# Kernel tuning notes

Hardware: AMD Instinct MI355X
Metric: run time of the kernel (lower is better)

## Reference

```python
import jax, jax.numpy as jnp
import numpy as np

B, N, K, D, H, FF, L, NH = 8, 50, 20, 3, 128, 2048, 3, 8
S = N * K
HD = H // NH


def setup_inputs() -> dict:
    key = jax.random.key(0)
    ks = jax.random.split(key, 16)
    visited = jax.random.uniform(ks[0], (B, S)) < 0.05
    # the single most-recent action per batch row (status flips 0 -> 1)
    action_idx = jax.random.randint(ks[1], (B,), 0, S)
    visited = visited.at[jnp.arange(B), action_idx].set(True)
    feats = jax.random.normal(ks[2], (B, S, D - 1)) * visited[:, :, None]
    state = jnp.concatenate([feats, visited[:, :, None].astype(jnp.float32)], axis=-1)
    prev_state = state.at[jnp.arange(B), action_idx, :].set(0.0)

    def w(k, shape, s=0.02):
        return jax.random.normal(k, shape, dtype=jnp.float32) * s

    return dict(
        prev_state=prev_state, state=state,
        W_pre=w(ks[3], (D, H)), b_pre=jnp.zeros(H),
        Wq=w(ks[4], (L, H, H)), bq=jnp.zeros((L, H)),
        Wk=w(ks[5], (L, H, H)), bk=jnp.zeros((L, H)),
        Wv=w(ks[6], (L, H, H)), bv=jnp.zeros((L, H)),
        Wo=w(ks[7], (L, H, H)), bo=jnp.zeros((L, H)),
        ln1_g=jnp.ones((L, H)), ln1_b=jnp.zeros((L, H)),
        Wff1=w(ks[8], (L, H, FF)), bff1=jnp.zeros((L, FF)),
        Wff2=w(ks[9], (L, FF, H)), bff2=jnp.zeros((L, H)),
        ln2_g=jnp.ones((L, H)), ln2_b=jnp.zeros((L, H)),
        W_comb=w(ks[10], (2 * H, H)), b_comb=jnp.zeros(H),
        W_dec=w(ks[11], (H, H)), b_dec=jnp.zeros(H),
        W_lin=w(ks[12], (S, S)), b_lin=jnp.zeros(S),
    )


def _layer_norm(x, g, b, eps=1e-5):
    m = jnp.mean(x, -1, keepdims=True)
    v = jnp.mean(jnp.square(x - m), -1, keepdims=True)
    return (x - m) * jax.lax.rsqrt(v + eps) * g + b


def _update_mask(state):
    # vectorized equivalent of the original Python-loop scatter mask
    status = state[:, :, -1] != 0                      # visited [B, S], S = K*N channel-major
    mask = status
    vis_kn = status.reshape(B, K, N)
    user_any = vis_kn.any(axis=1)                      # [B, N]: user visited on any channel
    mask = mask | jnp.broadcast_to(user_any[:, None, :], (B, K, N)).reshape(B, S)
    assigned = state.reshape(B, K, N, D).sum(-1) != 0  # [B, K, N]
    full = assigned.sum(-1) >= 2                       # [B, K]: channel already has 2 users
    mask = mask | jnp.broadcast_to(full[:, :, None], (B, K, N)).reshape(B, S)
    return mask


def reference(prev_state, state, W_pre, b_pre, Wq, bq, Wk, bk, Wv, bv, Wo, bo,
              ln1_g, ln1_b, Wff1, bff1, Wff2, bff2, ln2_g, ln2_b,
              W_comb, b_comb, W_dec, b_dec, W_lin, b_lin):
    mask = _update_mask(state)
    # exactly one status change per batch row (sequential RL step)
    diff = prev_state[:, :, -1] != state[:, :, -1]
    act_idx = jnp.argmax(diff, axis=1)                 # [B]

    x = state @ W_pre + b_pre                          # [B, S, H]
    scale = np.float32(1.0 / np.sqrt(HD))
    for i in range(L):  # 3 post-LN transformer encoder layers
        q = (x @ Wq[i] + bq[i]).reshape(B, S, NH, HD)
        k = (x @ Wk[i] + bk[i]).reshape(B, S, NH, HD)
        v = (x @ Wv[i] + bv[i]).reshape(B, S, NH, HD)
        att = jax.nn.softmax(jnp.einsum('bqhd,bkhd->bhqk', q, k) * scale, axis=-1)
        o = jnp.einsum('bhqk,bkhd->bqhd', att, v).reshape(B, S, H) @ Wo[i] + bo[i]
        x = _layer_norm(x + o, ln1_g[i], ln1_b[i])
        ff = jax.nn.relu(x @ Wff1[i] + bff1[i]) @ Wff2[i] + bff2[i]
        x = _layer_norm(x + ff, ln2_g[i], ln2_b[i])

    last = x[jnp.arange(B), act_idx]                   # [B, H]
    combined = jnp.concatenate([x.mean(axis=1), last], axis=-1)  # [B, 2H]
    g = combined @ W_comb + b_comb                     # [B, H]
    dec = x @ W_dec + b_dec                            # [B, S, H]
    scores = jnp.einsum('bsh,bh->bs', dec, g)          # [B, S]
    masked = scores @ W_lin + b_lin                    # Q-Learning head
    return jnp.where(mask, -jnp.inf, masked)
```

## Files before the change

### kernel.cpp

```cpp
#include <hip/hip_runtime.h>
#include <math.h>

#define Bb 8
#define Ss 1000
#define Kk 20
#define Nn 50
#define Dd 3
#define Hh 128
#define FFf 2048
#define Ll 3
#define NHh 8
#define HDd 16
#define ROWS (Bb*Ss)

#define SENTINEL -3.0e38f

typedef unsigned short ush;
typedef short short8 __attribute__((ext_vector_type(8)));
typedef short short4v __attribute__((ext_vector_type(4)));
typedef float f32x4 __attribute__((ext_vector_type(4)));

__device__ __forceinline__ ush f2b(float f) {
  unsigned x = __float_as_uint(f);
  return (ush)((x + 0x7fff + ((x >> 16) & 1)) >> 16);
}

__global__ __launch_bounds__(256) void mask_kernel(const float* __restrict__ state,
                                                   const float* __restrict__ prev_state,
                                                   int* __restrict__ mask, int* __restrict__ act_idx) {
  int b = blockIdx.x, tid = threadIdx.x;
  __shared__ unsigned char status[Ss], assigned[Ss], uany[Nn], fullk[Kk];
  __shared__ int act;
  if (tid == 0) act = 1 << 30;
  __syncthreads();
  for (int s = tid; s < Ss; s += 256) {
    const float* st = state + ((size_t)b * Ss + s) * Dd;
    float f2 = st[2];
    status[s] = (f2 != 0.f);
    assigned[s] = ((st[0] + st[1] + f2) != 0.f);
    float p2 = prev_state[((size_t)b * Ss + s) * Dd + 2];
    if (p2 != f2) atomicMin(&act, s);
  }
  __syncthreads();
  if (tid < Nn) {
    unsigned char a = 0;
    for (int k = 0; k < Kk; ++k) a |= status[k * Nn + tid];
    uany[tid] = a;
  } else if (tid >= 64 && tid < 64 + Kk) {
    int k = tid - 64, cnt = 0;
    for (int n = 0; n < Nn; ++n) cnt += assigned[k * Nn + n];
    fullk[k] = (cnt >= 2);
  }
  __syncthreads();
  for (int s = tid; s < Ss; s += 256)
    mask[b * Ss + s] = (int)(status[s] | uany[s % Nn] | fullk[s / Nn]);
  if (tid == 0) act_idx[b] = (act >= Ss) ? 0 : act;
}

__global__ __launch_bounds__(256) void pre_kernel(const float* __restrict__ state,
                                                  const float* __restrict__ W_pre,
                                                  const float* __restrict__ b_pre,
                                                  float* __restrict__ x, ush* __restrict__ xbf,
                                                  float* __restrict__ mpart) {
  int idx = blockIdx.x * 256 + threadIdx.x;
  if (idx >= ROWS * Hh) return;
  if (idx < Bb * Hh) mpart[idx] = 0.f;
  int row = idx >> 7, n = idx & 127;
  const float* st = state + (size_t)row * Dd;
  float v = b_pre[n] + st[0] * W_pre[n] + st[1] * W_pre[Hh + n] + st[2] * W_pre[2 * Hh + n];
  x[idx] = v;
  xbf[idx] = f2b(v);
}

#define TQKV 144
#define TWO  48
#define TFF1 768
#define TFF2 768
#define TWD  16
#define TBIAS 5
#define TTOT (TQKV+TWO+TFF1+TFF2+TWD+TBIAS)
__global__ __launch_bounds__(256) void transpose_prep(
    const float* __restrict__ Wq, const float* __restrict__ Wk, const float* __restrict__ Wv,
    const float* __restrict__ Wo, const float* __restrict__ Wff1, const float* __restrict__ Wff2,
    const float* __restrict__ bq, const float* __restrict__ bk, const float* __restrict__ bv,
    const float* __restrict__ W_dec,
    ush* __restrict__ wqkvT, ush* __restrict__ woT, ush* __restrict__ wff1T, ush* __restrict__ wff2T,
    float* __restrict__ bqkv, float* __restrict__ wdecT) {
  int t = blockIdx.x, tid = threadIdx.x;
  if (t >= TTOT - TBIAS) {
    int idx = (t - (TTOT - TBIAS)) * 256 + tid;
    if (idx < Ll * 384) {
      int l = idx / 384, c = idx % 384;
      bqkv[idx] = (c < 128) ? bq[l * Hh + c] : (c < 256 ? bk[l * Hh + c - 128] : bv[l * Hh + c - 256]);
    }
    return;
  }
  __shared__ float lf[32][33];
  int tr = tid >> 5, tc = tid & 31;
  const float* s; ush* d = nullptr; float* df = nullptr;
  int sp, dp;
  if (t < TQKV) {
    int l = t / 48, rem = t % 48, mat = rem / 16, tt = rem % 16;
    int ti = tt >> 2, tj = tt & 3;
    const float* m = (mat == 0) ? Wq : (mat == 1) ? Wk : Wv;
    s = m + (size_t)l * 16384 + (size_t)(ti * 32) * 128 + tj * 32; sp = 128;
    d = wqkvT + ((size_t)l * 384 + mat * 128 + tj * 32) * 128 + ti * 32; dp = 128;
  } else if (t < TQKV + TWO) {
    int r0 = t - TQKV; int l = r0 / 16, tt = r0 % 16, ti = tt >> 2, tj = tt & 3;
    s = Wo + (size_t)l * 16384 + (size_t)(ti * 32) * 128 + tj * 32; sp = 128;
    d = woT + ((size_t)l * 128 + tj * 32) * 128 + ti * 32; dp = 128;
  } else if (t < TQKV + TWO + TFF1) {
    int r0 = t - TQKV - TWO; int l = r0 / 256, tt = r0 % 256, ti = tt >> 6, tj = tt & 63;
    s = Wff1 + (size_t)l * 128 * 2048 + (size_t)(ti * 32) * 2048 + tj * 32; sp = 2048;
    d = wff1T + ((size_t)l * 2048 + tj * 32) * 128 + ti * 32; dp = 128;
  } else if (t < TQKV + TWO + TFF1 + TFF2) {
    int r0 = t - TQKV - TWO - TFF1; int l = r0 / 256, tt = r0 % 256, ti = tt >> 2, tj = tt & 3;
    s = Wff2 + (size_t)l * 2048 * 128 + (size_t)(ti * 32) * 128 + tj * 32; sp = 128;
    d = wff2T + ((size_t)l * 128 + tj * 32) * 2048 + ti * 32; dp = 2048;
  } else {
    int tt = t - TQKV - TWO - TFF1 - TFF2; int ti = tt >> 2, tj = tt & 3;
    s = W_dec + (size_t)(ti * 32) * 128 + tj * 32; sp = 128;
    df = wdecT + (size_t)(tj * 32) * 128 + ti * 32; dp = 128;
  }
#pragma unroll
  for (int p = 0; p < 4; ++p) {
    int r = tr + p * 8;
    lf[r][tc] = s[(size_t)r * sp + tc];
  }
  __syncthreads();
#pragma unroll
  for (int p = 0; p < 4; ++p) {
    int r = tr + p * 8;
    if (d) d[(size_t)r * dp + tc] = f2b(lf[tc][r]);
    else   df[(size_t)r * dp + tc] = lf[tc][r];
  }
}

#define LDP 40
template <int RELU, int QKVV>
__global__ __launch_bounds__(256) void gemm_mfma(const ush* __restrict__ A, const ush* __restrict__ Wt,
                                                 const float* __restrict__ bias, ush* __restrict__ out,
                                                 int N, int K, ush* __restrict__ vTout) {
  __shared__ ush As[2][64 * LDP];
  __shared__ ush Bs[2][64 * LDP];
  int tid = threadIdx.x;
  int lane = tid & 63, wid = tid >> 6;
  int wr = wid >> 1, wc = wid & 1;
  int m0 = blockIdx.y * 64, n0 = blockIdx.x * 64;
  int lrow = tid >> 2, lk = (tid & 3) << 3;
  int quad = lane >> 4, l16 = lane & 15, kb = quad << 3;

  const ush* Ap = A + (size_t)(m0 + lrow) * K + lk;
  const ush* Bp = Wt + (size_t)(n0 + lrow) * K + lk;

  f32x4 acc[2][2];
#pragma unroll
  for (int i = 0; i < 2; ++i)
#pragma unroll
    for (int j = 0; j < 2; ++j) acc[i][j] = (f32x4){0.f, 0.f, 0.f, 0.f};

  short8 pa = *(const short8*)Ap;
  short8 pb = *(const short8*)Bp;
  *(short8*)&As[0][lrow * LDP + lk] = pa;
  *(short8*)&Bs[0][lrow * LDP + lk] = pb;
  __syncthreads();

  int NT = K >> 5;
  for (int it = 0; it < NT; ++it) {
    int cur = it & 1;
    bool have = (it + 1 < NT);
    if (have) {
      pa = *(const short8*)(Ap + (it + 1) * 32);
      pb = *(const short8*)(Bp + (it + 1) * 32);
    }
    short8 a0 = *(short8*)&As[cur][(wr * 32 + l16) * LDP + kb];
    short8 a1 = *(short8*)&As[cur][(wr * 32 + 16 + l16) * LDP + kb];
    short8 b0 = *(short8*)&Bs[cur][(wc * 32 + l16) * LDP + kb];
    short8 b1 = *(short8*)&Bs[cur][(wc * 32 + 16 + l16) * LDP + kb];
    acc[0][0] = __builtin_amdgcn_mfma_f32_16x16x32_bf16(a0, b0, acc[0][0], 0, 0, 0);
    acc[0][1] = __builtin_amdgcn_mfma_f32_16x16x32_bf16(a0, b1, acc[0][1], 0, 0, 0);
    acc[1][0] = __builtin_amdgcn_mfma_f32_16x16x32_bf16(a1, b0, acc[1][0], 0, 0, 0);
    acc[1][1] = __builtin_amdgcn_mfma_f32_16x16x32_bf16(a1, b1, acc[1][1], 0, 0, 0);
    if (have) {
      *(short8*)&As[cur ^ 1][lrow * LDP + lk] = pa;
      *(short8*)&Bs[cur ^ 1][lrow * LDP + lk] = pb;
    }
    __syncthreads();
  }

#pragma unroll
  for (int i = 0; i < 2; ++i)
#pragma unroll
    for (int j = 0; j < 2; ++j) {
      int col = n0 + wc * 32 + j * 16 + l16;
      int rbase = m0 + wr * 32 + i * 16 + quad * 4;
      float bval = bias[col];
      if (QKVV && col >= 256) {
        int bb2 = rbase / 1000, qq = rbase - bb2 * 1000;
        short4v pk;
#pragma unroll
        for (int v = 0; v < 4; ++v) pk[v] = (short)f2b(acc[i][j][v] + bval);
        *(short4v*)&vTout[((size_t)(bb2 * 128 + (col - 256))) * 1024 + qq] = pk;
      } else {
#pragma unroll
        for (int v = 0; v < 4; ++v) {
          float o = acc[i][j][v] + bval;
          if (RELU) o = fmaxf(o, 0.f);
          out[(size_t)(rbase + v) * N + col] = f2b(o);
        }
      }
    }
}

#define XP 136
#define WP 72
template <int MEANOUT>
__global__ __launch_bounds__(512) void ff_fused(const ush* __restrict__ xin,
                                                const ush* __restrict__ w1T,
                                                const ush* __restrict__ w2T,
                                                const float* __restrict__ b1,
                                                const float* __restrict__ bias,
                                                const float* __restrict__ ln_g, const float* __restrict__ ln_b,
                                                float* __restrict__ x, ush* __restrict__ xbf,
                                                float* __restrict__ mpart) {
  __shared__ ush xs[32][XP];
  __shared__ ush W1L[2][64][XP];
  __shared__ ush W2L[2][128][WP];
  __shared__ ush hs[32][WP];
  __shared__ float pbias[128], pg[128], pb[128];
  __shared__ float red1[2][4][16], red2[2][4][16];

  int tid = threadIdx.x, lane = tid & 63, w = tid >> 6;
  int f = w & 3, xr = w >> 2;
  int l16 = lane & 15, quad = lane >> 4, kb = quad * 8;
  int m0 = blockIdx.x * 32;

  { int row = tid >> 4, seg = (tid & 15) << 3;
    *(short8*)&xs[row][seg] = *(const short8*)(xin + (size_t)(m0 + row) * 128 + seg); }
  if (tid < 128) { pbias[tid] = bias[tid]; pg[tid] = ln_g[tid]; pb[tid] = ln_b[tid]; }

  int w1row = tid >> 3, w1seg = (tid & 7) << 3;
  int w2row = tid >> 2, w2seg = (tid & 3) << 4;

  short8 r0a, r0b, r0c, r0d, r1a, r1b, r1c, r1d;

  r0a = *(const short8*)(w1T + (size_t)w1row * 128 + w1seg);
  r0b = *(const short8*)(w1T + (size_t)w1row * 128 + w1seg + 64);
  r0c = *(const short8*)(w2T + (size_t)w2row * 2048 + w2seg);
  r0d = *(const short8*)(w2T + (size_t)w2row * 2048 + w2seg + 8);
  *(short8*)&W1L[0][w1row][w1seg] = r0a;
  *(short8*)&W1L[0][w1row][w1seg + 64] = r0b;
  *(short8*)&W2L[0][w2row][w2seg] = r0c;
  *(short8*)&W2L[0][w2row][w2seg + 8] = r0d;
  r1a = *(const short8*)(w1T + (size_t)(64 + w1row) * 128 + w1seg);
  r1b = *(const short8*)(w1T + (size_t)(64 + w1row) * 128 + w1seg + 64);
  r1c = *(const short8*)(w2T + (size_t)w2row * 2048 + 64 + w2seg);
  r1d = *(const short8*)(w2T + (size_t)w2row * 2048 + 64 + w2seg + 8);
  __syncthreads();

  f32x4 acc[2];
  acc[0] = (f32x4){0.f, 0.f, 0.f, 0.f};
  acc[1] = (f32x4){0.f, 0.f, 0.f, 0.f};
  const f32x4 zero4 = (f32x4){0.f, 0.f, 0.f, 0.f};

  for (int k = 0; k < 16; ++k) {
    int c0 = 2 * k, c1 = 2 * k + 1;
    if (c0 + 2 < 32) {
      r0a = *(const short8*)(w1T + (size_t)((c0 + 2) * 64 + w1row) * 128 + w1seg);
      r0b = *(const short8*)(w1T + (size_t)((c0 + 2) * 64 + w1row) * 128 + w1seg + 64);
      r0c = *(const short8*)(w2T + (size_t)w2row * 2048 + (c0 + 2) * 64 + w2seg);
      r0d = *(const short8*)(w2T + (size_t)w2row * 2048 + (c0 + 2) * 64 + w2seg + 8);
    }
    {
      f32x4 hacc = zero4;
#pragma unroll
      for (int ks = 0; ks < 4; ++ks) {
        short8 a = *(short8*)&W1L[0][f * 16 + l16][ks * 32 + kb];
        short8 b = *(short8*)&xs[xr * 16 + l16][ks * 32 + kb];
        hacc = __builtin_amdgcn_mfma_f32_16x16x32_bf16(a, b, hacc, 0, 0, 0);
      }
      int ffb = c0 * 64 + f * 16 + quad * 4;
      float4 bv1 = *(const float4*)(b1 + ffb);
      float h0 = fmaxf(hacc[0] + bv1.x, 0.f);
      float h1 = fmaxf(hacc[1] + bv1.y, 0.f);
      float h2 = fmaxf(hacc[2] + bv1.z, 0.f);
      float h3 = fmaxf(hacc[3] + bv1.w, 0.f);
      unsigned lo, hi;
      asm("v_cvt_pk_bf16_f32 %0, %1, %2" : "=v"(lo) : "v"(h0), "v"(h1));
      asm("v_cvt_pk_bf16_f32 %0, %1, %2" : "=v"(hi) : "v"(h2), "v"(h3));
      *(uint2*)&hs[xr * 16 + l16][f * 16 + quad * 4] = make_uint2(lo, hi);
    }
    __syncthreads();
#pragma unroll
    for (int ks = 0; ks < 2; ++ks) {
      short8 a = *(short8*)&hs[xr * 16 + l16][ks * 32 + kb];
#pragma unroll
      for (int j = 0; j < 2; ++j) {
        short8 b = *(short8*)&W2L[0][f * 32 + j * 16 + l16][ks * 32 + kb];
        acc[j] = __builtin_amdgcn_mfma_f32_16x16x32_bf16(a, b, acc[j], 0, 0, 0);
      }
    }
    *(short8*)&W1L[1][w1row][w1seg] = r1a;
    *(short8*)&W1L[1][w1row][w1seg + 64] = r1b;
    *(short8*)&W2L[1][w2row][w2seg] = r1c;
    *(short8*)&W2L[1][w2row][w2seg + 8] = r1d;
    __syncthreads();
    if (c1 + 2 < 32) {
      r1a = *(const short8*)(w1T + (size_t)((c1 + 2) * 64 + w1row) * 128 + w1seg);
      r1b = *(const short8*)(w1T + (size_t)((c1 + 2) * 64 + w1row) * 128 + w1seg + 64);
      r1c = *(const short8*)(w2T + (size_t)w2row * 2048 + (c1 + 2) * 64 + w2seg);
      r1d = *(const short8*)(w2T + (size_t)w2row * 2048 + (c1 + 2) * 64 + w2seg + 8);
    }
    {
      f32x4 hacc = zero4;
#pragma unroll
      for (int ks = 0; ks < 4; ++ks) {
        short8 a = *(short8*)&W1L[1][f * 16 + l16][ks * 32 + kb];
        short8 b = *(short8*)&xs[xr * 16 + l16][ks * 32 + kb];
        hacc = __builtin_amdgcn_mfma_f32_16x16x32_bf16(a, b, hacc, 0, 0, 0);
      }
      int ffb = c1 * 64 + f * 16 + quad * 4;
      float4 bv1 = *(const float4*)(b1 + ffb);
      float h0 = fmaxf(hacc[0] + bv1.x, 0.f);
      float h1 = fmaxf(hacc[1] + bv1.y, 0.f);
      float h2 = fmaxf(hacc[2] + bv1.z, 0.f);
      float h3 = fmaxf(hacc[3] + bv1.w, 0.f);
      unsigned lo, hi;
      asm("v_cvt_pk_bf16_f32 %0, %1, %2" : "=v"(lo) : "v"(h0), "v"(h1));
      asm("v_cvt_pk_bf16_f32 %0, %1, %2" : "=v"(hi) : "v"(h2), "v"(h3));
      *(uint2*)&hs[xr * 16 + l16][f * 16 + quad * 4] = make_uint2(lo, hi);
    }
    __syncthreads();
#pragma unroll
    for (int ks = 0; ks < 2; ++ks) {
      short8 a = *(short8*)&hs[xr * 16 + l16][ks * 32 + kb];
#pragma unroll
      for (int j = 0; j < 2; ++j) {
        short8 b = *(short8*)&W2L[1][f * 32 + j * 16 + l16][ks * 32 + kb];
        acc[j] = __builtin_amdgcn_mfma_f32_16x16x32_bf16(a, b, acc[j], 0, 0, 0);
      }
    }
    if (c1 + 1 < 32) {
      *(short8*)&W1L[0][w1row][w1seg] = r0a;
      *(short8*)&W1L[0][w1row][w1seg + 64] = r0b;
      *(short8*)&W2L[0][w2row][w2seg] = r0c;
      *(short8*)&W2L[0][w2row][w2seg + 8] = r0d;
    }
    __syncthreads();
  }

  float v[2][4], s1[4] = {0.f, 0.f, 0.f, 0.f}, s2[4] = {0.f, 0.f, 0.f, 0.f};
#pragma unroll
  for (int j = 0; j < 2; ++j) {
    int col = f * 32 + j * 16 + l16;
#pragma unroll
    for (int r = 0; r < 4; ++r) {
      int row = m0 + xr * 16 + quad * 4 + r;
      float vv = acc[j][r] + pbias[col] + x[(size_t)row * Hh + col];
      v[j][r] = vv; s1[r] += vv; s2[r] += vv * vv;
    }
  }
#pragma unroll
  for (int m = 1; m <= 8; m <<= 1) {
#pragma unroll
    for (int r = 0; r < 4; ++r) { s1[r] += __shfl_xor(s1[r], m); s2[r] += __shfl_xor(s2[r], m); }
  }
  if (l16 == 0) {
#pragma unroll
    for (int r = 0; r < 4; ++r) {
      red1[xr][f][quad * 4 + r] = s1[r];
      red2[xr][f][quad * 4 + r] = s2[r];
    }
  }
  __syncthreads();
  float osum[2] = {0.f, 0.f};
#pragma unroll
  for (int r = 0; r < 4; ++r) {
    int qr = quad * 4 + r;
    float t1 = red1[xr][0][qr] + red1[xr][1][qr] + red1[xr][2][qr] + red1[xr][3][qr];
    float t2 = red2[xr][0][qr] + red2[xr][1][qr] + red2[xr][2][qr] + red2[xr][3][qr];
    float mean = t1 * (1.f / 128.f);
    float var = t2 * (1.f / 128.f) - mean * mean;
    float rstd = rsqrtf(var + 1e-5f);
    int row = m0 + xr * 16 + qr;
#pragma unroll
    for (int j = 0; j < 2; ++j) {
      int col = f * 32 + j * 16 + l16;
      float o = (v[j][r] - mean) * rstd * pg[col] + pb[col];
      size_t gi = (size_t)row * Hh + col;
      x[gi] = o; xbf[gi] = f2b(o);
      if (MEANOUT) osum[j] += o;
    }
  }
  if (MEANOUT) {
    int gb = (m0 + xr * 16 + quad * 4) / 1000;
#pragma unroll
    for (int j = 0; j < 2; ++j)
      atomicAdd(&mpart[gb * 128 + f * 32 + j * 16 + l16], osum[j]);
  }
}

#define F2P 72
__global__ __launch_bounds__(256) void gemm_ln16(const ush* __restrict__ A,
                                                 const ush* __restrict__ Wt,
                                                 const float* __restrict__ bias,
                                                 const float* __restrict__ ln_g, const float* __restrict__ ln_b,
                                                 float* __restrict__ x, ush* __restrict__ xbf) {
  __shared__ ush As[2][16 * F2P];
  __shared__ ush Bs[2][128 * F2P];
  __shared__ float red1[4][16], red2[4][16];
  __shared__ float pbias[128], pg[128], pb[128];

  int tid = threadIdx.x, lane = tid & 63, w = tid >> 6;
  int l16 = lane & 15, quad = lane >> 4, kb = quad * 8;
  int m0 = blockIdx.x * 16;
  if (tid < 128) { pbias[tid] = bias[tid]; pg[tid] = ln_g[tid]; pb[tid] = ln_b[tid]; }

  f32x4 acc[2];
  acc[0] = (f32x4){0.f, 0.f, 0.f, 0.f};
  acc[1] = (f32x4){0.f, 0.f, 0.f, 0.f};

  int srow = tid >> 3, slk = (tid & 7) << 3;
  const ush* Ap = A + (size_t)(m0 + srow) * 128 + slk;
  const ush* Bp = Wt + (size_t)srow * 128 + slk;

  short8 pa;
  short8 pbr[4];
  if (tid < 128) pa = *(const short8*)Ap;
#pragma unroll
  for (int rep = 0; rep < 4; ++rep)
    pbr[rep] = *(const short8*)(Bp + (size_t)rep * 32 * 128);
  if (tid < 128) *(short8*)&As[0][srow * F2P + slk] = pa;
#pragma unroll
  for (int rep = 0; rep < 4; ++rep)
    *(short8*)&Bs[0][(rep * 32 + srow) * F2P + slk] = pbr[rep];
  __syncthreads();

#pragma unroll
  for (int it = 0; it < 2; ++it) {
    if (it == 0) {
      if (tid < 128) pa = *(const short8*)(Ap + 64);
#pragma unroll
      for (int rep = 0; rep < 4; ++rep)
        pbr[rep] = *(const short8*)(Bp + (size_t)rep * 32 * 128 + 64);
    }
#pragma unroll
    for (int kk = 0; kk < 2; ++kk) {
      short8 a = *(short8*)&As[it][l16 * F2P + kk * 32 + kb];
#pragma unroll
      for (int j = 0; j < 2; ++j) {
        short8 b = *(short8*)&Bs[it][(w * 32 + j * 16 + l16) * F2P + kk * 32 + kb];
        acc[j] = __builtin_amdgcn_mfma_f32_16x16x32_bf16(a, b, acc[j], 0, 0, 0);
      }
    }
    if (it == 0) {
      if (tid < 128) *(short8*)&As[1][srow * F2P + slk] = pa;
#pragma unroll
      for (int rep = 0; rep < 4; ++rep)
        *(short8*)&Bs[1][(rep * 32 + srow) * F2P + slk] = pbr[rep];
    }
    __syncthreads();
  }

  float v[2][4], s1[4] = {0.f, 0.f, 0.f, 0.f}, s2[4] = {0.f, 0.f, 0.f, 0.f};
#pragma unroll
  for (int j = 0; j < 2; ++j) {
    int col = w * 32 + j * 16 + l16;
#pragma unroll
    for (int r = 0; r < 4; ++r) {
      int row = m0 + quad * 4 + r;
      float vv = acc[j][r] + pbias[col] + x[(size_t)row * Hh + col];
      v[j][r] = vv; s1[r] += vv; s2[r] += vv * vv;
    }
  }
#pragma unroll
  for (int m = 1; m <= 8; m <<= 1) {
#pragma unroll
    for (int r = 0; r < 4; ++r) { s1[r] += __shfl_xor(s1[r], m); s2[r] += __shfl_xor(s2[r], m); }
  }
  if (l16 == 0) {
#pragma unroll
    for (int r = 0; r < 4; ++r) {
      red1[w][quad * 4 + r] = s1[r];
      red2[w][quad * 4 + r] = s2[r];
    }
  }
  __syncthreads();
#pragma unroll
  for (int r = 0; r < 4; ++r) {
    int qr = quad * 4 + r;
    float t1 = red1[0][qr] + red1[1][qr] + red1[2][qr] + red1[3][qr];
    float t2 = red2[0][qr] + red2[1][qr] + red2[2][qr] + red2[3][qr];
    float mean = t1 * (1.f / 128.f);
    float var = t2 * (1.f / 128.f) - mean * mean;
    float rstd = rsqrtf(var + 1e-5f);
    int row = m0 + qr;
#pragma unroll
    for (int j = 0; j < 2; ++j) {
      int col = w * 32 + j * 16 + l16;
      float o = (v[j][r] - mean) * rstd * pg[col] + pb[col];
      size_t gi = (size_t)row * Hh + col;
      x[gi] = o; xbf[gi] = f2b(o);
    }
  }
}

__global__ __launch_bounds__(256) void attn_mfma(const ush* __restrict__ qkv,
                                                 const ush* __restrict__ vT,
                                                 ush* __restrict__ attn_o) {
  int blk = blockIdx.x;
  int local = blk >> 3;
  int bh = ((blk & 7) << 3) | (local >> 4);
  int qt = local & 15;
  int b = bh >> 3, h = bh & 7;
  int qbase = qt * 64;
  int tid = threadIdx.x, lane = tid & 63, w = tid >> 6;
  int l16 = lane & 15, quad = lane >> 4, kb = quad * 8;

  __shared__ ush Ks[2][64][40];
  __shared__ ush Vs[2][16][72];
  __shared__ ush Pb[4][16][72];

  if (tid < 128) {
    int row = tid >> 1, g = tid & 1;
    *(short8*)&Ks[0][row][16 + g * 8] = (short8){0, 0, 0, 0, 0, 0, 0, 0};
    *(short8*)&Ks[1][row][16 + g * 8] = (short8){0, 0, 0, 0, 0, 0, 0, 0};
  }

  int qrow = qbase + w * 16 + l16; if (qrow >= Ss) qrow = Ss - 1;
  short8 aq = *(const short8*)(qkv + (size_t)(b * Ss + qrow) * 384 + h * HDd + kb);

  int srow = tid >> 1, sg = tid & 1;
  int sd = (tid - 128) >> 3, skg = (tid - 128) & 7;
  const ush* kbase = qkv + (size_t)b * Ss * 384 + 128 + h * HDd;
  const ush* vbase = vT + (size_t)(b * 128 + h * 16) * 1024;

  if (tid < 128) {
    short8 s8 = (short8){0, 0, 0, 0, 0, 0, 0, 0};
    if (srow < Ss) s8 = *(const short8*)(kbase + (size_t)srow * 384 + sg * 8);
    *(short8*)&Ks[0][srow][sg * 8] = s8;
  } else {
    *(short8*)&Vs[0][sd][skg * 8] = *(const short8*)(vbase + (size_t)sd * 1024 + skg * 8);
  }
  __syncthreads();

  const short one_b = (short)0x3F80;
  const short8 ones = (short8){one_b, one_b, one_b, one_b, one_b, one_b, one_b, one_b};
  f32x4 acc_pv = (f32x4){0.f, 0.f, 0.f, 0.f};
  f32x4 acc_l = (f32x4){0.f, 0.f, 0.f, 0.f};
  const f32x4 zero4 = (f32x4){0.f, 0.f, 0.f, 0.f};

  for (int it = 0; it < 16; ++it) {
    int k0 = it * 64;
    int cur = it & 1, nxt = cur ^ 1;
    bool have = (it + 1 < 16);

    short8 gk, gv;
    if (have) {
      if (tid < 128) {
        gk = (short8){0, 0, 0, 0, 0, 0, 0, 0};
        int key = k0 + 64 + srow;
        if (key < Ss) gk = *(const short8*)(kbase + (size_t)key * 384 + sg * 8);
      } else {
        gv = *(const short8*)(vbase + (size_t)sd * 1024 + k0 + 64 + skg * 8);
      }
    }

    bool tail = (k0 + 64 > Ss);
#pragma unroll
    for (int kn = 0; kn < 4; ++kn) {
      short8 ak = *(short8*)&Ks[cur][kn * 16 + l16][kb];
      f32x4 s = __builtin_amdgcn_mfma_f32_16x16x32_bf16(ak, aq, zero4, 0, 0, 0);
      float p0 = __expf(s[0] * 0.25f);
      float p1 = __expf(s[1] * 0.25f);
      float p2 = __expf(s[2] * 0.25f);
      float p3 = __expf(s[3] * 0.25f);
      if (tail) {
        int keyb = k0 + kn * 16 + quad * 4;
        if (keyb + 0 >= Ss) p0 = 0.f;
        if (keyb + 1 >= Ss) p1 = 0.f;
        if (keyb + 2 >= Ss) p2 = 0.f;
        if (keyb + 3 >= Ss) p3 = 0.f;
      }
      unsigned lo, hi;
      asm("v_cvt_pk_bf16_f32 %0, %1, %2" : "=v"(lo) : "v"(p0), "v"(p1));
      asm("v_cvt_pk_bf16_f32 %0, %1, %2" : "=v"(hi) : "v"(p2), "v"(p3));
      *(uint2*)&Pb[w][l16][kn * 16 + quad * 4] = make_uint2(lo, hi);
    }

    short8 pa0 = *(short8*)&Pb[w][l16][kb];
    short8 pa1 = *(short8*)&Pb[w][l16][32 + kb];
    short8 vb0 = *(short8*)&Vs[cur][l16][kb];
    short8 vb1 = *(short8*)&Vs[cur][l16][32 + kb];
    acc_pv = __builtin_amdgcn_mfma_f32_16x16x32_bf16(pa0, vb0, acc_pv, 0, 0, 0);
    acc_pv = __builtin_amdgcn_mfma_f32_16x16x32_bf16(pa1, vb1, acc_pv, 0, 0, 0);
    acc_l = __builtin_amdgcn_mfma_f32_16x16x32_bf16(pa0, ones, acc_l, 0, 0, 0);
    acc_l = __builtin_amdgcn_mfma_f32_16x16x32_bf16(pa1, ones, acc_l, 0, 0, 0);

    if (have) {
      if (tid < 128) *(short8*)&Ks[nxt][srow][sg * 8] = gk;
      else *(short8*)&Vs[nxt][sd][skg * 8] = gv;
    }
    __syncthreads();
  }

#pragma unroll
  for (int r = 0; r < 4; ++r) {
    int q = qbase + w * 16 + quad * 4 + r;
    if (q < Ss)
      attn_o[((size_t)(b * Ss + q)) * Hh + h * HDd + l16] = f2b(acc_pv[r] / acc_l[r]);
  }
}

__global__ __launch_bounds__(128) void ghc_kernel(const float* __restrict__ x, const float* __restrict__ mpart,
                                                  const int* __restrict__ act_idx,
                                                  const float* __restrict__ W_comb, const float* __restrict__ b_comb,
                                                  const float* __restrict__ wdecT, const float* __restrict__ b_dec,
                                                  float* __restrict__ h, float* __restrict__ cb) {
  int b = blockIdx.x, n = threadIdx.x;
  __shared__ float cs[2 * Hh], gs[Hh], red[2];
  cs[n] = mpart[b * Hh + n] * (1.f / Ss);
  cs[Hh + n] = x[((size_t)b * Ss + act_idx[b]) * Hh + n];
  __syncthreads();
  float acc = b_comb[n];
  for (int j = 0; j < 2 * Hh; ++j) acc += cs[j] * W_comb[(size_t)j * Hh + n];
  gs[n] = acc;
  __syncthreads();
  float hv = 0.f;
  for (int c = 0; c < Hh; ++c) hv += wdecT[(size_t)c * Hh + n] * gs[c];
  h[b * Hh + n] = hv;
  float t = b_dec[n] * gs[n];
  for (int off = 32; off; off >>= 1) t += __shfl_down(t, off);
  if ((n & 63) == 0) red[n >> 6] = t;
  __syncthreads();
  if (n == 0) cb[b] = red[0] + red[1];
}

__global__ __launch_bounds__(256) void scores_kernel(const float* __restrict__ x, const float* __restrict__ h,
                                                     const float* __restrict__ cb, float* __restrict__ scores) {
  int wid = threadIdx.x >> 6, lane = threadIdx.x & 63;
  int row = blockIdx.x * 4 + wid;
  if (row >= ROWS) return;
  int b = row / Ss;
  const float* xr = x + (size_t)row * Hh;
  const float* hb = h + b * Hh;
  float s = xr[lane] * hb[lane] + xr[lane + 64] * hb[lane + 64];
  for (int off = 32; off; off >>= 1) s += __shfl_down(s, off);
  if (lane == 0) scores[row] = s + cb[b];
}

__global__ __launch_bounds__(256) void final_part(const float* __restrict__ scores,
                                                  const float* __restrict__ W_lin,
                                                  float* __restrict__ fpart) {
  int spc = blockIdx.x, kc = blockIdx.y;
  int tid = threadIdx.x;
  __shared__ float ss[8][125];
  for (int i = tid; i < 8 * 125; i += 256) {
    int bb = i / 125, s = i - bb * 125;
    ss[bb][s] = scores[bb * Ss + kc * 125 + s];
  }
  __syncthreads();
  if (tid < 250) {
    int sp = spc * 250 + tid;
    float acc[8];
#pragma unroll
    for (int bb = 0; bb < 8; ++bb) acc[bb] = 0.f;
    const float* wl = &W_lin[(size_t)(kc * 125) * Ss + sp];
#pragma unroll 5
    for (int s = 0; s < 125; ++s) {
      float wv = wl[(size_t)s * Ss];
#pragma unroll
      for (int bb = 0; bb < 8; ++bb) acc[bb] = fmaf(ss[bb][s], wv, acc[bb]);
    }
#pragma unroll
    for (int bb = 0; bb < 8; ++bb)
      fpart[((size_t)kc * Bb + bb) * Ss + sp] = acc[bb];
  }
}

__global__ __launch_bounds__(256) void final_combine(const float* __restrict__ fpart,
                                                     const float* __restrict__ b_lin,
                                                     const int* __restrict__ mask,
                                                     float* __restrict__ out) {
  int b = blockIdx.y;
  int sp = blockIdx.x * 256 + threadIdx.x;
  if (sp >= Ss) return;
  float acc = b_lin[sp];
#pragma unroll
  for (int kc = 0; kc < 8; ++kc) acc += fpart[((size_t)kc * Bb + b) * Ss + sp];
  out[b * Ss + sp] = mask[b * Ss + sp] ? SENTINEL : acc;
}

extern "C" void kernel_launch(void* const* d_in, const int* in_sizes, int n_in,
                              void* d_out, int out_size, void* d_ws, size_t ws_size,
                              hipStream_t stream) {
  const float* prev_state = (const float*)d_in[0];
  const float* state = (const float*)d_in[1];
  const float* W_pre = (const float*)d_in[2];
  const float* b_pre = (const float*)d_in[3];
  const float* Wq = (const float*)d_in[4];
  const float* bq = (const float*)d_in[5];
  const float* Wk = (const float*)d_in[6];
  const float* bk = (const float*)d_in[7];
  const float* Wv = (const float*)d_in[8];
  const float* bv = (const float*)d_in[9];
  const float* Wo = (const float*)d_in[10];
  const float* bo = (const float*)d_in[11];
  const float* ln1_g = (const float*)d_in[12];
  const float* ln1_b = (const float*)d_in[13];
  const float* Wff1 = (const float*)d_in[14];
  const float* bff1 = (const float*)d_in[15];
  const float* Wff2 = (const float*)d_in[16];
  const float* bff2 = (const float*)d_in[17];
  const float* ln2_g = (const float*)d_in[18];
  const float* ln2_b = (const float*)d_in[19];
  const float* W_comb = (const float*)d_in[20];
  const float* b_comb = (const float*)d_in[21];
  const float* W_dec = (const float*)d_in[22];
  const float* b_dec = (const float*)d_in[23];
  const float* W_lin = (const float*)d_in[24];
  const float* b_lin = (const float*)d_in[25];

  char* wsp = (char*)d_ws;
  auto alloc = [&](size_t bytes) { char* p = wsp; wsp += (bytes + 255) & ~(size_t)255; return p; };
  int* mask = (int*)alloc(ROWS * 4);
  int* act = (int*)alloc(Bb * 4);
  ush* wqkvT = (ush*)alloc((size_t)Ll * 384 * 128 * 2);
  ush* woT = (ush*)alloc((size_t)Ll * 128 * 128 * 2);
  ush* wff1T = (ush*)alloc((size_t)Ll * 2048 * 128 * 2);
  ush* wff2T = (ush*)alloc((size_t)Ll * 128 * 2048 * 2);
  float* bqkv = (float*)alloc((size_t)Ll * 384 * 4);
  float* wdecT = (float*)alloc((size_t)Hh * Hh * 4);
  float* x = (float*)alloc((size_t)ROWS * Hh * 4);
  ush* xbf = (ush*)alloc((size_t)ROWS * Hh * 2);
  ush* qkv_bf = (ush*)alloc((size_t)ROWS * 384 * 2);
  ush* vT = (ush*)alloc((size_t)Bb * 128 * 1024 * 2);
  ush* attn_ob = (ush*)alloc((size_t)ROWS * Hh * 2);
  float* mpart = (float*)alloc((size_t)Bb * Hh * 4);
  float* hbuf = (float*)alloc((size_t)Bb * Hh * 4);
  float* cb = (float*)alloc((size_t)Bb * 4);
  float* scores = (float*)alloc((size_t)ROWS * 4);
  float* fpart = (float*)alloc((size_t)8 * Bb * Ss * 4);

  transpose_prep<<<dim3(TTOT), 256, 0, stream>>>(Wq, Wk, Wv, Wo, Wff1, Wff2, bq, bk, bv, W_dec,
                                                 wqkvT, woT, wff1T, wff2T, bqkv, wdecT);
  mask_kernel<<<Bb, 256, 0, stream>>>(state, prev_state, mask, act);
  pre_kernel<<<dim3((ROWS * Hh + 255) / 256), 256, 0, stream>>>(state, W_pre, b_pre, x, xbf, mpart);

  for (int l = 0; l < Ll; ++l) {
    gemm_mfma<0, 1><<<dim3(384 / 64, ROWS / 64), 256, 0, stream>>>(
        xbf, wqkvT + (size_t)l * 384 * 128, bqkv + l * 384, qkv_bf, 384, 128, vT);
    attn_mfma<<<dim3(1024), 256, 0, stream>>>(qkv_bf, vT, attn_ob);
    gemm_ln16<<<dim3(ROWS / 16), 256, 0, stream>>>(
        attn_ob, woT + (size_t)l * 128 * 128, bo + l * Hh, ln1_g + l * Hh, ln1_b + l * Hh, x, xbf);
    if (l == Ll - 1)
      ff_fused<1><<<dim3(ROWS / 32), 512, 0, stream>>>(
          xbf, wff1T + (size_t)l * 2048 * 128, wff2T + (size_t)l * 128 * 2048,
          bff1 + l * FFf, bff2 + l * Hh, ln2_g + l * Hh, ln2_b + l * Hh, x, xbf, mpart);
    else
      ff_fused<0><<<dim3(ROWS / 32), 512, 0, stream>>>(
          xbf, wff1T + (size_t)l * 2048 * 128, wff2T + (size_t)l * 128 * 2048,
          bff1 + l * FFf, bff2 + l * Hh, ln2_g + l * Hh, ln2_b + l * Hh, x, xbf, mpart);
  }

  ghc_kernel<<<Bb, 128, 0, stream>>>(x, mpart, act, W_comb, b_comb, wdecT, b_dec, hbuf, cb);
  scores_kernel<<<dim3(ROWS / 4), 256, 0, stream>>>(x, hbuf, cb, scores);
  final_part<<<dim3(4, 8), 256, 0, stream>>>(scores, W_lin, fpart);
  final_combine<<<dim3(4, Bb), 256, 0, stream>>>(fpart, b_lin, mask, (float*)d_out);
}
```

Measured before the change: 357.0 us.

## Software-pipeline FF1 and FF2 stages with double-buffered hidden tile

Restructures the fused feed-forward loop so the first GEMM for chunk c+1 is computed before the second GEMM consumes chunk c. The hidden activation tile in shared memory is double-buffered to allow this. The aim is to let the two MFMA phases interleave and remove one barrier per chunk, so each barrier now covers both the weight staging and the hidden tile. The cost is a prologue, extra shared memory, and tighter ordering requirements between buffers.

```diff
diff --git a/kernel.cpp b/kernel.cpp
--- a/kernel.cpp
+++ b/kernel.cpp
@@ -226,7 +226,7 @@
   __shared__ ush xs[32][XP];
   __shared__ ush W1L[2][64][XP];
   __shared__ ush W2L[2][128][WP];
-  __shared__ ush hs[32][WP];
+  __shared__ ush hs[2][32][WP];
   __shared__ float pbias[128], pg[128], pb[128];
   __shared__ float red1[2][4][16], red2[2][4][16];
 
@@ -263,6 +263,26 @@
   acc[1] = (f32x4){0.f, 0.f, 0.f, 0.f};
   const f32x4 zero4 = (f32x4){0.f, 0.f, 0.f, 0.f};
 
+  {
+    f32x4 hacc = zero4;
+#pragma unroll
+    for (int ks = 0; ks < 4; ++ks) {
+      short8 a = *(short8*)&W1L[0][f * 16 + l16][ks * 32 + kb];
+      short8 b = *(short8*)&xs[xr * 16 + l16][ks * 32 + kb];
+      hacc = __builtin_amdgcn_mfma_f32_16x16x32_bf16(a, b, hacc, 0, 0, 0);
+    }
+    int ffb = f * 16 + quad * 4;
+    float4 bv1 = *(const float4*)(b1 + ffb);
+    float h0 = fmaxf(hacc[0] + bv1.x, 0.f);
+    float h1 = fmaxf(hacc[1] + bv1.y, 0.f);
+    float h2 = fmaxf(hacc[2] + bv1.z, 0.f);
+    float h3 = fmaxf(hacc[3] + bv1.w, 0.f);
+    unsigned lo, hi;
+    asm("v_cvt_pk_bf16_f32 %0, %1, %2" : "=v"(lo) : "v"(h0), "v"(h1));
+    asm("v_cvt_pk_bf16_f32 %0, %1, %2" : "=v"(hi) : "v"(h2), "v"(h3));
+    *(uint2*)&hs[0][xr * 16 + l16][f * 16 + quad * 4] = make_uint2(lo, hi);
+  }
+
   for (int k = 0; k < 16; ++k) {
     int c0 = 2 * k, c1 = 2 * k + 1;
     if (c0 + 2 < 32) {
@@ -271,15 +291,20 @@
       r0c = *(const short8*)(w2T + (size_t)w2row * 2048 + (c0 + 2) * 64 + w2seg);
       r0d = *(const short8*)(w2T + (size_t)w2row * 2048 + (c0 + 2) * 64 + w2seg + 8);
     }
+    *(short8*)&W1L[1][w1row][w1seg] = r1a;
+    *(short8*)&W1L[1][w1row][w1seg + 64] = r1b;
+    *(short8*)&W2L[1][w2row][w2seg] = r1c;
+    *(short8*)&W2L[1][w2row][w2seg + 8] = r1d;
+    __syncthreads();
     {
       f32x4 hacc = zero4;
 #pragma unroll
       for (int ks = 0; ks < 4; ++ks) {
-        short8 a = *(short8*)&W1L[0][f * 16 + l16][ks * 32 + kb];
+        short8 a = *(short8*)&W1L[1][f * 16 + l16][ks * 32 + kb];
         short8 b = *(short8*)&xs[xr * 16 + l16][ks * 32 + kb];
         hacc = __builtin_amdgcn_mfma_f32_16x16x32_bf16(a, b, hacc, 0, 0, 0);
       }
-      int ffb = c0 * 64 + f * 16 + quad * 4;
+      int ffb = (c0 + 1) * 64 + f * 16 + quad * 4;
       float4 bv1 = *(const float4*)(b1 + ffb);
       float h0 = fmaxf(hacc[0] + bv1.x, 0.f);
       float h1 = fmaxf(hacc[1] + bv1.y, 0.f);
@@ -288,22 +313,17 @@
       unsigned lo, hi;
       asm("v_cvt_pk_bf16_f32 %0, %1, %2" : "=v"(lo) : "v"(h0), "v"(h1));
       asm("v_cvt_pk_bf16_f32 %0, %1, %2" : "=v"(hi) : "v"(h2), "v"(h3));
-      *(uint2*)&hs[xr * 16 + l16][f * 16 + quad * 4] = make_uint2(lo, hi);
-    }
-    __syncthreads();
+      *(uint2*)&hs[1][xr * 16 + l16][f * 16 + quad * 4] = make_uint2(lo, hi);
+    }
 #pragma unroll
     for (int ks = 0; ks < 2; ++ks) {
-      short8 a = *(short8*)&hs[xr * 16 + l16][ks * 32 + kb];
+      short8 a = *(short8*)&hs[0][xr * 16 + l16][ks * 32 + kb];
 #pragma unroll
       for (int j = 0; j < 2; ++j) {
         short8 b = *(short8*)&W2L[0][f * 32 + j * 16 + l16][ks * 32 + kb];
         acc[j] = __builtin_amdgcn_mfma_f32_16x16x32_bf16(a, b, acc[j], 0, 0, 0);
       }
     }
-    *(short8*)&W1L[1][w1row][w1seg] = r1a;
-    *(short8*)&W1L[1][w1row][w1seg + 64] = r1b;
-    *(short8*)&W2L[1][w2row][w2seg] = r1c;
-    *(short8*)&W2L[1][w2row][w2seg + 8] = r1d;
     __syncthreads();
     if (c1 + 2 < 32) {
       r1a = *(const short8*)(w1T + (size_t)((c1 + 2) * 64 + w1row) * 128 + w1seg);
@@ -311,15 +331,22 @@
       r1c = *(const short8*)(w2T + (size_t)w2row * 2048 + (c1 + 2) * 64 + w2seg);
       r1d = *(const short8*)(w2T + (size_t)w2row * 2048 + (c1 + 2) * 64 + w2seg + 8);
     }
-    {
+    if (c1 + 1 < 32) {
+      *(short8*)&W1L[0][w1row][w1seg] = r0a;
+      *(short8*)&W1L[0][w1row][w1seg + 64] = r0b;
+      *(short8*)&W2L[0][w2row][w2seg] = r0c;
+      *(short8*)&W2L[0][w2row][w2seg + 8] = r0d;
+    }
+    __syncthreads();
+    if (c1 + 1 < 32) {
       f32x4 hacc = zero4;
 #pragma unroll
       for (int ks = 0; ks < 4; ++ks) {
-        short8 a = *(short8*)&W1L[1][f * 16 + l16][ks * 32 + kb];
+        short8 a = *(short8*)&W1L[0][f * 16 + l16][ks * 32 + kb];
         short8 b = *(short8*)&xs[xr * 16 + l16][ks * 32 + kb];
         hacc = __builtin_amdgcn_mfma_f32_16x16x32_bf16(a, b, hacc, 0, 0, 0);
       }
-      int ffb = c1 * 64 + f * 16 + quad * 4;
+      int ffb = (c1 + 1) * 64 + f * 16 + quad * 4;
       float4 bv1 = *(const float4*)(b1 + ffb);
       float h0 = fmaxf(hacc[0] + bv1.x, 0.f);
       float h1 = fmaxf(hacc[1] + bv1.y, 0.f);
@@ -328,23 +355,16 @@
       unsigned lo, hi;
       asm("v_cvt_pk_bf16_f32 %0, %1, %2" : "=v"(lo) : "v"(h0), "v"(h1));
       asm("v_cvt_pk_bf16_f32 %0, %1, %2" : "=v"(hi) : "v"(h2), "v"(h3));
-      *(uint2*)&hs[xr * 16 + l16][f * 16 + quad * 4] = make_uint2(lo, hi);
-    }
-    __syncthreads();
+      *(uint2*)&hs[0][xr * 16 + l16][f * 16 + quad * 4] = make_uint2(lo, hi);
+    }
 #pragma unroll
     for (int ks = 0; ks < 2; ++ks) {
-      short8 a = *(short8*)&hs[xr * 16 + l16][ks * 32 + kb];
+      short8 a = *(short8*)&hs[1][xr * 16 + l16][ks * 32 + kb];
 #pragma unroll
       for (int j = 0; j < 2; ++j) {
         short8 b = *(short8*)&W2L[1][f * 32 + j * 16 + l16][ks * 32 + kb];
         acc[j] = __builtin_amdgcn_mfma_f32_16x16x32_bf16(a, b, acc[j], 0, 0, 0);
       }
-    }
-    if (c1 + 1 < 32) {
-      *(short8*)&W1L[0][w1row][w1seg] = r0a;
-      *(short8*)&W1L[0][w1row][w1seg + 64] = r0b;
-      *(short8*)&W2L[0][w2row][w2seg] = r0c;
-      *(short8*)&W2L[0][w2row][w2seg + 8] = r0d;
     }
     __syncthreads();
   }
```

New measurement: 363.5 us. About the same (+1.8%).

## Load FF weights and x fragments directly into registers, drop LDS staging

Applied to the files above, without the earlier changes.

The fused FFN kernel no longer stages W1/W2 tiles and the x tile through shared memory. Each wave loads its MFMA operand fragments straight from global memory into registers, prefetching the next W1 chunk one iteration ahead. The hidden-activation buffer is double-buffered by chunk parity, so each chunk needs one barrier instead of two. This removes LDS traffic and barriers, but each wave now issues its own global loads, so different waves fetch the same weights repeatedly and more latency is exposed.

```diff
diff --git a/kernel.cpp b/kernel.cpp
--- a/kernel.cpp
+++ b/kernel.cpp
@@ -212,7 +212,6 @@
     }
 }
 
-#define XP 136
 #define WP 72
 template <int MEANOUT>
 __global__ __launch_bounds__(512) void ff_fused(const ush* __restrict__ xin,
@@ -223,10 +222,7 @@
                                                 const float* __restrict__ ln_g, const float* __restrict__ ln_b,
                                                 float* __restrict__ x, ush* __restrict__ xbf,
                                                 float* __restrict__ mpart) {
-  __shared__ ush xs[32][XP];
-  __shared__ ush W1L[2][64][XP];
-  __shared__ ush W2L[2][128][WP];
-  __shared__ ush hs[32][WP];
+  __shared__ ush hs[2][32][WP];
   __shared__ float pbias[128], pg[128], pb[128];
   __shared__ float red1[2][4][16], red2[2][4][16];
 
@@ -234,52 +230,42 @@
   int f = w & 3, xr = w >> 2;
   int l16 = lane & 15, quad = lane >> 4, kb = quad * 8;
   int m0 = blockIdx.x * 32;
-
-  { int row = tid >> 4, seg = (tid & 15) << 3;
-    *(short8*)&xs[row][seg] = *(const short8*)(xin + (size_t)(m0 + row) * 128 + seg); }
   if (tid < 128) { pbias[tid] = bias[tid]; pg[tid] = ln_g[tid]; pb[tid] = ln_b[tid]; }
 
-  int w1row = tid >> 3, w1seg = (tid & 7) << 3;
-  int w2row = tid >> 2, w2seg = (tid & 3) << 4;
-
-  short8 r0a, r0b, r0c, r0d, r1a, r1b, r1c, r1d;
-
-  r0a = *(const short8*)(w1T + (size_t)w1row * 128 + w1seg);
-  r0b = *(const short8*)(w1T + (size_t)w1row * 128 + w1seg + 64);
-  r0c = *(const short8*)(w2T + (size_t)w2row * 2048 + w2seg);
-  r0d = *(const short8*)(w2T + (size_t)w2row * 2048 + w2seg + 8);
-  *(short8*)&W1L[0][w1row][w1seg] = r0a;
-  *(short8*)&W1L[0][w1row][w1seg + 64] = r0b;
-  *(short8*)&W2L[0][w2row][w2seg] = r0c;
-  *(short8*)&W2L[0][w2row][w2seg + 8] = r0d;
-  r1a = *(const short8*)(w1T + (size_t)(64 + w1row) * 128 + w1seg);
-  r1b = *(const short8*)(w1T + (size_t)(64 + w1row) * 128 + w1seg + 64);
-  r1c = *(const short8*)(w2T + (size_t)w2row * 2048 + 64 + w2seg);
-  r1d = *(const short8*)(w2T + (size_t)w2row * 2048 + 64 + w2seg + 8);
-  __syncthreads();
+  short8 xfrag[4];
+  const ush* xrow = xin + (size_t)(m0 + xr * 16 + l16) * 128 + kb;
+#pragma unroll
+  for (int ks = 0; ks < 4; ++ks) xfrag[ks] = *(const short8*)(xrow + ks * 32);
+
+  const ush* w1p = w1T + (size_t)(f * 16 + l16) * 128 + kb;
+  const ush* w2pA = w2T + (size_t)(f * 32 + l16) * 2048 + kb;
+  const ush* w2pB = w2T + (size_t)(f * 32 + 16 + l16) * 2048 + kb;
+
+  short8 w1cur[4], w1nxt[4], w2c0, w2c1, w2c2, w2c3;
+#pragma unroll
+  for (int ks = 0; ks < 4; ++ks) w1cur[ks] = *(const short8*)(w1p + ks * 32);
 
   f32x4 acc[2];
   acc[0] = (f32x4){0.f, 0.f, 0.f, 0.f};
   acc[1] = (f32x4){0.f, 0.f, 0.f, 0.f};
   const f32x4 zero4 = (f32x4){0.f, 0.f, 0.f, 0.f};
 
-  for (int k = 0; k < 16; ++k) {
-    int c0 = 2 * k, c1 = 2 * k + 1;
-    if (c0 + 2 < 32) {
-      r0a = *(const short8*)(w1T + (size_t)((c0 + 2) * 64 + w1row) * 128 + w1seg);
-      r0b = *(const short8*)(w1T + (size_t)((c0 + 2) * 64 + w1row) * 128 + w1seg + 64);
-      r0c = *(const short8*)(w2T + (size_t)w2row * 2048 + (c0 + 2) * 64 + w2seg);
-      r0d = *(const short8*)(w2T + (size_t)w2row * 2048 + (c0 + 2) * 64 + w2seg + 8);
-    }
+  for (int c = 0; c < 32; ++c) {
+    w2c0 = *(const short8*)(w2pA + c * 64);
+    w2c1 = *(const short8*)(w2pA + c * 64 + 32);
+    w2c2 = *(const short8*)(w2pB + c * 64);
+    w2c3 = *(const short8*)(w2pB + c * 64 + 32);
+    if (c + 1 < 32) {
+#pragma unroll
+      for (int ks = 0; ks < 4; ++ks)
+        w1nxt[ks] = *(const short8*)(w1p + (size_t)(c + 1) * 8192 + ks * 32);
+    }
+    f32x4 hacc = zero4;
+#pragma unroll
+    for (int ks = 0; ks < 4; ++ks)
+      hacc = __builtin_amdgcn_mfma_f32_16x16x32_bf16(w1cur[ks], xfrag[ks], hacc, 0, 0, 0);
     {
-      f32x4 hacc = zero4;
-#pragma unroll
-      for (int ks = 0; ks < 4; ++ks) {
-        short8 a = *(short8*)&W1L[0][f * 16 + l16][ks * 32 + kb];
-        short8 b = *(short8*)&xs[xr * 16 + l16][ks * 32 + kb];
-        hacc = __builtin_amdgcn_mfma_f32_16x16x32_bf16(a, b, hacc, 0, 0, 0);
-      }
-      int ffb = c0 * 64 + f * 16 + quad * 4;
+      int ffb = c * 64 + f * 16 + quad * 4;
       float4 bv1 = *(const float4*)(b1 + ffb);
       float h0 = fmaxf(hacc[0] + bv1.x, 0.f);
       float h1 = fmaxf(hacc[1] + bv1.y, 0.f);
@@ -288,65 +274,19 @@
       unsigned lo, hi;
       asm("v_cvt_pk_bf16_f32 %0, %1, %2" : "=v"(lo) : "v"(h0), "v"(h1));
       asm("v_cvt_pk_bf16_f32 %0, %1, %2" : "=v"(hi) : "v"(h2), "v"(h3));
-      *(uint2*)&hs[xr * 16 + l16][f * 16 + quad * 4] = make_uint2(lo, hi);
+      *(uint2*)&hs[c & 1][xr * 16 + l16][f * 16 + quad * 4] = make_uint2(lo, hi);
     }
     __syncthreads();
 #pragma unroll
     for (int ks = 0; ks < 2; ++ks) {
-      short8 a = *(short8*)&hs[xr * 16 + l16][ks * 32 + kb];
-#pragma unroll
-      for (int j = 0; j < 2; ++j) {
-        short8 b = *(short8*)&W2L[0][f * 32 + j * 16 + l16][ks * 32 + kb];
-        acc[j] = __builtin_amdgcn_mfma_f32_16x16x32_bf16(a, b, acc[j], 0, 0, 0);
-      }
-    }
-    *(short8*)&W1L[1][w1row][w1seg] = r1a;
-    *(short8*)&W1L[1][w1row][w1seg + 64] = r1b;
-    *(short8*)&W2L[1][w2row][w2seg] = r1c;
-    *(short8*)&W2L[1][w2row][w2seg + 8] = r1d;
-    __syncthreads();
-    if (c1 + 2 < 32) {
-      r1a = *(const short8*)(w1T + (size_t)((c1 + 2) * 64 + w1row) * 128 + w1seg);
-      r1b = *(const short8*)(w1T + (size_t)((c1 + 2) * 64 + w1row) * 128 + w1seg + 64);
-      r1c = *(const short8*)(w2T + (size_t)w2row * 2048 + (c1 + 2) * 64 + w2seg);
-      r1d = *(const short8*)(w2T + (size_t)w2row * 2048 + (c1 + 2) * 64 + w2seg + 8);
-    }
-    {
-      f32x4 hacc = zero4;
-#pragma unroll
-      for (int ks = 0; ks < 4; ++ks) {
-        short8 a = *(short8*)&W1L[1][f * 16 + l16][ks * 32 + kb];
-        short8 b = *(short8*)&xs[xr * 16 + l16][ks * 32 + kb];
-        hacc = __builtin_amdgcn_mfma_f32_16x16x32_bf16(a, b, hacc, 0, 0, 0);
-      }
-      int ffb = c1 * 64 + f * 16 + quad * 4;
-      float4 bv1 = *(const float4*)(b1 + ffb);
-      float h0 = fmaxf(hacc[0] + bv1.x, 0.f);
-      float h1 = fmaxf(hacc[1] + bv1.y, 0.f);
-      float h2 = fmaxf(hacc[2] + bv1.z, 0.f);
-      float h3 = fmaxf(hacc[3] + bv1.w, 0.f);
-      unsigned lo, hi;
-      asm("v_cvt_pk_bf16_f32 %0, %1, %2" : "=v"(lo) : "v"(h0), "v"(h1));
-      asm("v_cvt_pk_bf16_f32 %0, %1, %2" : "=v"(hi) : "v"(h2), "v"(h3));
-      *(uint2*)&hs[xr * 16 + l16][f * 16 + quad * 4] = make_uint2(lo, hi);
-    }
-    __syncthreads();
-#pragma unroll
-    for (int ks = 0; ks < 2; ++ks) {
-      short8 a = *(short8*)&hs[xr * 16 + l16][ks * 32 + kb];
-#pragma unroll
-      for (int j = 0; j < 2; ++j) {
-        short8 b = *(short8*)&W2L[1][f * 32 + j * 16 + l16][ks * 32 + kb];
-        acc[j] = __builtin_amdgcn_mfma_f32_16x16x32_bf16(a, b, acc[j], 0, 0, 0);
-      }
-    }
-    if (c1 + 1 < 32) {
-      *(short8*)&W1L[0][w1row][w1seg] = r0a;
-      *(short8*)&W1L[0][w1row][w1seg + 64] = r0b;
-      *(short8*)&W2L[0][w2row][w2seg] = r0c;
-      *(short8*)&W2L[0][w2row][w2seg + 8] = r0d;
-    }
-    __syncthreads();
+      short8 a = *(short8*)&hs[c & 1][xr * 16 + l16][ks * 32 + kb];
+      short8 b0 = (ks == 0) ? w2c0 : w2c1;
+      short8 b1v = (ks == 0) ? w2c2 : w2c3;
+      acc[0] = __builtin_amdgcn_mfma_f32_16x16x32_bf16(a, b0, acc[0], 0, 0, 0);
+      acc[1] = __builtin_amdgcn_mfma_f32_16x16x32_bf16(a, b1v, acc[1], 0, 0, 0);
+    }
+#pragma unroll
+    for (int ks = 0; ks < 4; ++ks) w1cur[ks] = w1nxt[ks];
   }
 
   float v[2][4], s1[4] = {0.f, 0.f, 0.f, 0.f}, s2[4] = {0.f, 0.f, 0.f, 0.f};
```

Result: slower. 460.3 us (+28.9%).
